# Kernel tuning notes

Measured on AMD Instinct MI355X. Metric: run time of the kernel, lower is better.

## Reference

```python
import jax, jax.numpy as jnp
import numpy as np

T, N, G = 4, 100000, 128
R, B, K = 4, 4096, 32
I = 128


def setup_inputs() -> dict:
    key = jax.random.key(0)
    k1, k2, k3, k4 = jax.random.split(key, 4)
    embeddings = jax.random.normal(k1, (T, N, G), dtype=jnp.float32)
    neighbor_idx = jax.random.randint(k2, (T, R, B, K), 0, N, dtype=jnp.int32)
    neighbor_mask = jax.random.randint(k3, (T, R, B, K), 0, 2).astype(jnp.bool_)
    # xavier_uniform per relation weight [G, I]
    limit = float(np.sqrt(6.0 / (G + I)))
    weights = jax.random.uniform(k4, (R, G, I), dtype=jnp.float32, minval=-limit, maxval=limit)
    return {
        "embeddings": embeddings,
        "weights": weights,
        "neighbor_idx": neighbor_idx,
        "neighbor_mask": neighbor_mask,
        "train_year": T,
    }


def reference(embeddings, weights, neighbor_idx, neighbor_mask, train_year):
    # embeddings: [T, N, G]; neighbor_idx/mask: [T, R, B, K]; weights: [R, G, I]
    m = neighbor_mask.astype(embeddings.dtype)               # [T,R,B,K]
    year = jnp.arange(embeddings.shape[0])[:, None, None, None]
    gathered = embeddings[year, neighbor_idx]                 # [T,R,B,K,G]
    summed = jnp.einsum('trbkg,trbk->trbg', gathered, m)      # masked neighbor sum
    cnt = jnp.maximum(m.sum(-1), 1.0)                         # empty list -> divide by 1 (zeros row)
    mean = summed / cnt[..., None]                            # [T,R,B,G]
    out = jnp.einsum('trbg,rgi->tbi', mean, weights)          # per-relation matmul, sum over R
    return out.reshape(-1, train_year, weights.shape[-1])     # raw flat reshape, as in original
```

## Files before the change

### kernel.cpp

```cpp
#include <hip/hip_runtime.h>

#define T_ 4
#define N_ 100000
#define G_ 128
#define R_ 4
#define B_ 4096
#define K_ 32
#define I_ 128
#define BB 8

__global__ __launch_bounds__(256) void static_influence_kernel(
    const float* __restrict__ E,
    const float* __restrict__ W,
    const int*   __restrict__ idx,
    const int*   __restrict__ msk,
    float*       __restrict__ out)
{
    const int tid = threadIdx.x;
    const int blk = blockIdx.x;
    const int t   = blk / (B_ / BB);
    const int b0  = (blk % (B_ / BB)) * BB;

    __shared__ float mean_s[BB][G_];
    __shared__ int   idxc_s[BB * K_];
    __shared__ int   cnt_s[BB];

    const int wave = tid >> 6;
    const int lane = tid & 63;
    const int half = lane >> 5;
    const int gl   = lane & 31;
    const int bbg  = 2 * wave + half;

    const int iset = tid >> 7;
    const int i    = tid & 127;

    const float* __restrict__ Et = E + (size_t)t * N_ * G_;

    float acc0 = 0.f, acc1 = 0.f, acc2 = 0.f, acc3 = 0.f;

    for (int r = 0; r < R_; ++r) {
        {
            const int base = ((t * R_ + r) * B_ + b0) * K_;
            const int  v   = idx[base + tid];
            const bool act = (msk[base + tid] != 0);
            const unsigned long long bal = __ballot(act);
            int rank = __popcll(bal & ((1ULL << lane) - 1));
            if (half) rank -= __popcll(bal & 0xFFFFFFFFULL);
            const int row = tid >> 5;
            if (act) idxc_s[row * K_ + rank] = v;
            if ((lane & 31) == 0)
                cnt_s[row] = __popcll((bal >> (half * 32)) & 0xFFFFFFFFULL);
        }
        __syncthreads();

        const int myc    = cnt_s[bbg];
        const int rowbas = bbg * K_;
        float4 s4 = make_float4(0.f, 0.f, 0.f, 0.f);
        for (int k0 = 0; k0 < K_; k0 += 8) {
            if (k0 >= myc) break;
            int ids[8];
#pragma unroll
            for (int j = 0; j < 8; ++j) {
                int kk = k0 + j;
                kk = (kk < myc) ? kk : (myc - 1);
                ids[j] = idxc_s[rowbas + kk];
            }
            float4 e[8];
#pragma unroll
            for (int j = 0; j < 8; ++j)
                e[j] = *reinterpret_cast<const float4*>(Et + (size_t)ids[j] * G_ + gl * 4);
#pragma unroll
            for (int j = 0; j < 8; ++j) {
                if (k0 + j < myc) {
                    s4.x += e[j].x;  s4.y += e[j].y;
                    s4.z += e[j].z;  s4.w += e[j].w;
                }
            }
        }
        const float inv = 1.0f / fmaxf((float)myc, 1.0f);
        *reinterpret_cast<float4*>(&mean_s[bbg][gl * 4]) =
            make_float4(s4.x * inv, s4.y * inv, s4.z * inv, s4.w * inv);
        __syncthreads();

        const float* __restrict__ Wr = W + r * G_ * I_;
        const int bbm = iset * 4;
#pragma unroll 2
        for (int g = 0; g < G_; g += 4) {
            const float w0 = Wr[(g + 0) * I_ + i];
            const float w1 = Wr[(g + 1) * I_ + i];
            const float w2 = Wr[(g + 2) * I_ + i];
            const float w3 = Wr[(g + 3) * I_ + i];
            const float4 m0 = *reinterpret_cast<const float4*>(&mean_s[bbm + 0][g]);
            const float4 m1 = *reinterpret_cast<const float4*>(&mean_s[bbm + 1][g]);
            const float4 m2 = *reinterpret_cast<const float4*>(&mean_s[bbm + 2][g]);
            const float4 m3 = *reinterpret_cast<const float4*>(&mean_s[bbm + 3][g]);
            acc0 += m0.x * w0 + m0.y * w1 + m0.z * w2 + m0.w * w3;
            acc1 += m1.x * w0 + m1.y * w1 + m1.z * w2 + m1.w * w3;
            acc2 += m2.x * w0 + m2.y * w1 + m2.z * w2 + m2.w * w3;
            acc3 += m3.x * w0 + m3.y * w1 + m3.z * w2 + m3.w * w3;
        }
        __syncthreads();
    }

    const size_t ob = ((size_t)t * B_ + b0 + iset * 4) * I_ + i;
    out[ob + 0 * I_] = acc0;
    out[ob + 1 * I_] = acc1;
    out[ob + 2 * I_] = acc2;
    out[ob + 3 * I_] = acc3;
}

extern "C" void kernel_launch(void* const* d_in, const int* in_sizes, int n_in,
                              void* d_out, int out_size, void* d_ws, size_t ws_size,
                              hipStream_t stream) {
    const float* E   = (const float*)d_in[0];
    const float* W   = (const float*)d_in[1];
    const int*   idx = (const int*)d_in[2];
    const int*   msk = (const int*)d_in[3];
    float* out = (float*)d_out;

    dim3 grid(T_ * (B_ / BB));
    dim3 block(256);
    hipLaunchKernelGGL(static_influence_kernel, grid, block, 0, stream,
                       E, W, idx, msk, out);
}
```

Before: 366.3 us.

## Software-pipeline next relation's neighbor gather with current relation's matmul

```diff
diff --git a/kernel.cpp b/kernel.cpp
--- a/kernel.cpp
+++ b/kernel.cpp
@@ -21,15 +21,13 @@
     const int t   = blk / (B_ / BB);
     const int b0  = (blk % (B_ / BB)) * BB;
 
-    __shared__ float mean_s[BB][G_];
+    __shared__ float mean_s[2][BB][G_];
     __shared__ int   idxc_s[BB * K_];
-    __shared__ int   cnt_s[BB];
 
-    const int wave = tid >> 6;
     const int lane = tid & 63;
     const int half = lane >> 5;
     const int gl   = lane & 31;
-    const int bbg  = 2 * wave + half;
+    const int row  = tid >> 5;
 
     const int iset = tid >> 7;
     const int i    = tid & 127;
@@ -38,68 +36,110 @@
 
     float acc0 = 0.f, acc1 = 0.f, acc2 = 0.f, acc3 = 0.f;
 
-    for (int r = 0; r < R_; ++r) {
-        {
-            const int base = ((t * R_ + r) * B_ + b0) * K_;
-            const int  v   = idx[base + tid];
-            const bool act = (msk[base + tid] != 0);
-            const unsigned long long bal = __ballot(act);
-            int rank = __popcll(bal & ((1ULL << lane) - 1));
-            if (half) rank -= __popcll(bal & 0xFFFFFFFFULL);
-            const int row = tid >> 5;
-            if (act) idxc_s[row * K_ + rank] = v;
-            if ((lane & 31) == 0)
-                cnt_s[row] = __popcll((bal >> (half * 32)) & 0xFFFFFFFFULL);
+    auto stage_idx = [&](int r) -> int {
+        const int base = ((t * R_ + r) * B_ + b0) * K_;
+        const int  v   = idx[base + tid];
+        const bool act = (msk[base + tid] != 0);
+        const unsigned long long bal = __ballot(act);
+        int rank = __popcll(bal & ((1ULL << lane) - 1));
+        if (half) rank -= __popcll(bal & 0xFFFFFFFFULL);
+        if (act) idxc_s[row * K_ + rank] = v;
+        return (int)__popcll((bal >> (half * 32)) & 0xFFFFFFFFULL);
+    };
+
+    auto gather8 = [&](int k0, int myc, float4& s4) {
+        int ids[8];
+#pragma unroll
+        for (int j = 0; j < 8; ++j) {
+            int kk = k0 + j;
+            kk = (kk < myc) ? kk : (myc - 1);
+            ids[j] = idxc_s[row * K_ + kk];
         }
-        __syncthreads();
+        float4 e[8];
+#pragma unroll
+        for (int j = 0; j < 8; ++j)
+            e[j] = *reinterpret_cast<const float4*>(Et + (size_t)ids[j] * G_ + gl * 4);
+#pragma unroll
+        for (int j = 0; j < 8; ++j)
+            if (k0 + j < myc) {
+                s4.x += e[j].x;  s4.y += e[j].y;
+                s4.z += e[j].z;  s4.w += e[j].w;
+            }
+    };
 
-        const int myc    = cnt_s[bbg];
-        const int rowbas = bbg * K_;
+    float4 pe[8];
+
+    auto issue8 = [&](int myc) {
+        int ids[8];
+#pragma unroll
+        for (int j = 0; j < 8; ++j) {
+            int kk = (j < myc) ? j : (myc - 1);
+            ids[j] = idxc_s[row * K_ + kk];
+        }
+#pragma unroll
+        for (int j = 0; j < 8; ++j)
+            pe[j] = *reinterpret_cast<const float4*>(Et + (size_t)ids[j] * G_ + gl * 4);
+    };
+    auto consume8 = [&](int myc, float4& s4) {
+#pragma unroll
+        for (int j = 0; j < 8; ++j)
+            if (j < myc) {
+                s4.x += pe[j].x;  s4.y += pe[j].y;
+                s4.z += pe[j].z;  s4.w += pe[j].w;
+            }
+    };
+
+    {
+        const int myc = stage_idx(0);
         float4 s4 = make_float4(0.f, 0.f, 0.f, 0.f);
         for (int k0 = 0; k0 < K_; k0 += 8) {
             if (k0 >= myc) break;
-            int ids[8];
-#pragma unroll
-            for (int j = 0; j < 8; ++j) {
-                int kk = k0 + j;
-                kk = (kk < myc) ? kk : (myc - 1);
-                ids[j] = idxc_s[rowbas + kk];
-            }
-            float4 e[8];
-#pragma unroll
-            for (int j = 0; j < 8; ++j)
-                e[j] = *reinterpret_cast<const float4*>(Et + (size_t)ids[j] * G_ + gl * 4);
-#pragma unroll
-            for (int j = 0; j < 8; ++j) {
-                if (k0 + j < myc) {
-                    s4.x += e[j].x;  s4.y += e[j].y;
-                    s4.z += e[j].z;  s4.w += e[j].w;
-                }
-            }
+            gather8(k0, myc, s4);
         }
         const float inv = 1.0f / fmaxf((float)myc, 1.0f);
-        *reinterpret_cast<float4*>(&mean_s[bbg][gl * 4]) =
+        *reinterpret_cast<float4*>(&mean_s[0][row][gl * 4]) =
             make_float4(s4.x * inv, s4.y * inv, s4.z * inv, s4.w * inv);
+    }
+
+    for (int r = 0; r < R_; ++r) {
         __syncthreads();
+
+        int nmyc = 0;
+        if (r + 1 < R_) {
+            nmyc = stage_idx(r + 1);
+            if (nmyc > 0) issue8(nmyc);
+        }
 
         const float* __restrict__ Wr = W + r * G_ * I_;
         const int bbm = iset * 4;
+        const float (*__restrict__ ms)[G_] = mean_s[r & 1];
 #pragma unroll 2
         for (int g = 0; g < G_; g += 4) {
             const float w0 = Wr[(g + 0) * I_ + i];
             const float w1 = Wr[(g + 1) * I_ + i];
             const float w2 = Wr[(g + 2) * I_ + i];
             const float w3 = Wr[(g + 3) * I_ + i];
-            const float4 m0 = *reinterpret_cast<const float4*>(&mean_s[bbm + 0][g]);
-            const float4 m1 = *reinterpret_cast<const float4*>(&mean_s[bbm + 1][g]);
-            const float4 m2 = *reinterpret_cast<const float4*>(&mean_s[bbm + 2][g]);
-            const float4 m3 = *reinterpret_cast<const float4*>(&mean_s[bbm + 3][g]);
+            const float4 m0 = *reinterpret_cast<const float4*>(&ms[bbm + 0][g]);
+            const float4 m1 = *reinterpret_cast<const float4*>(&ms[bbm + 1][g]);
+            const float4 m2 = *reinterpret_cast<const float4*>(&ms[bbm + 2][g]);
+            const float4 m3 = *reinterpret_cast<const float4*>(&ms[bbm + 3][g]);
             acc0 += m0.x * w0 + m0.y * w1 + m0.z * w2 + m0.w * w3;
             acc1 += m1.x * w0 + m1.y * w1 + m1.z * w2 + m1.w * w3;
             acc2 += m2.x * w0 + m2.y * w1 + m2.z * w2 + m2.w * w3;
             acc3 += m3.x * w0 + m3.y * w1 + m3.z * w2 + m3.w * w3;
         }
-        __syncthreads();
+
+        if (r + 1 < R_) {
+            float4 n4 = make_float4(0.f, 0.f, 0.f, 0.f);
+            if (nmyc > 0) consume8(nmyc, n4);
+            for (int k0 = 8; k0 < K_; k0 += 8) {
+                if (k0 >= nmyc) break;
+                gather8(k0, nmyc, n4);
+            }
+            const float inv = 1.0f / fmaxf((float)nmyc, 1.0f);
+            *reinterpret_cast<float4*>(&mean_s[(r + 1) & 1][row][gl * 4]) =
+                make_float4(n4.x * inv, n4.y * inv, n4.z * inv, n4.w * inv);
+        }
     }
 
     const size_t ob = ((size_t)t * B_ + b0 + iset * 4) * I_ + i;
```

Result: no change. 365.4 us (-0.3%).
